# Optimization experiments

Measured on AMD Instinct MI355X. Metric: run time of the kernel, lower is better.

The kernel has to match this reference:

```python
import jax, jax.numpy as jnp
import numpy as np

T, N = 20, 32768          # seq_length, numNodes
D_IN, D_EMB, D_H, D_OUT = 2, 64, 128, 5


def setup_inputs() -> dict:
    key = jax.random.key(0)
    ks = jax.random.split(key, 12)
    s = 0.05
    return {
        "nodes": jax.random.normal(ks[0], (T, N, D_IN), jnp.float32),
        "present_mask": jax.random.randint(ks[1], (T, N), 0, 2).astype(bool),
        "hidden_states": jax.random.normal(ks[2], (N, D_H), jnp.float32),
        "cell_states": jax.random.normal(ks[3], (N, D_H), jnp.float32),
        "W_embed": jax.random.normal(ks[4], (D_IN, D_EMB), jnp.float32) * s,
        "b_embed": jnp.zeros((D_EMB,), jnp.float32),
        "W_ih": jax.random.normal(ks[5], (D_EMB, 4 * D_H), jnp.float32) * s,
        "b_ih": jnp.zeros((4 * D_H,), jnp.float32),
        "W_hh": jax.random.normal(ks[6], (D_H, 4 * D_H), jnp.float32) * s,
        "b_hh": jnp.zeros((4 * D_H,), jnp.float32),
        "W_out": jax.random.normal(ks[7], (D_H, D_OUT), jnp.float32) * s,
        "b_out": jnp.zeros((D_OUT,), jnp.float32),
    }


def reference(nodes, present_mask, hidden_states, cell_states,
              W_embed, b_embed, W_ih, b_ih, W_hh, b_hh, W_out, b_out):
    # Per-frame: gather present nodes -> embed+ReLU (dropout=eval identity)
    # -> LSTMCell -> scatter h/c/output back. Gather+scatter is expressed as
    # a masked update, which is mathematically identical.
    def step(carry, frame):
        h, c = carry
        x, mask = frame                      # x: [N,2], mask: [N]
        emb = jax.nn.relu(x @ W_embed + b_embed)              # [N,Demb]
        gates = emb @ W_ih + b_ih + h @ W_hh + b_hh           # [N,4H]
        i, f, g, o = jnp.split(gates, 4, axis=-1)             # torch order
        i, f, o = jax.nn.sigmoid(i), jax.nn.sigmoid(f), jax.nn.sigmoid(o)
        g = jnp.tanh(g)
        c_new = f * c + i * g
        h_new = o * jnp.tanh(c_new)
        m = mask[:, None]
        h = jnp.where(m, h_new, h)
        c = jnp.where(m, c_new, c)
        out = jnp.where(m, h_new @ W_out + b_out, 0.0)        # absent -> zeros
        return (h, c), out

    (h_fin, c_fin), outputs = jax.lax.scan(
        step, (hidden_states, cell_states), (nodes, present_mask))
    return outputs, h_fin, c_fin                              # [T,N,5],[N,H],[N,H]
```

## Files before the change

### kernel.cpp

```cpp
#include <hip/hip_runtime.h>
#include <cstddef>


typedef __attribute__((ext_vector_type(8))) short  s16x8;
typedef __attribute__((ext_vector_type(4))) float  f32x4;

namespace {
constexpr int T_STEPS = 20;
constexpr int NN      = 32768;
constexpr int D_EMB   = 64;
constexpr int D_H     = 128;
constexpr int D_OUT   = 5;
constexpr int G4      = 512;
constexpr int MT      = 64;
constexpr int BLOCK   = 512;
constexpr int GRID    = NN / MT;
constexpr int WP_ELEMS   = 8 * 4 * 6 * 64 * 8;
constexpr int WOUT_ELEMS = 4 * 64 * 8;
constexpr float LOG2E = 1.4426950408889634f;
constexpr float AM4   = -4.0f * LOG2E;
constexpr float AP2   =  2.0f * LOG2E;
constexpr float CINV  = 0.34657359027997264f;
constexpr size_t OFF_H = (size_t)T_STEPS * NN * D_OUT;
constexpr size_t OFF_C = OFF_H + (size_t)NN * D_H;
}

__device__ __forceinline__ unsigned short f2bf(float x) {
    unsigned u = __float_as_uint(x);
    u = (u + 0x7FFFu + ((u >> 16) & 1u)) >> 16;
    return (unsigned short)u;
}
__device__ __forceinline__ unsigned short f2bf_hw(float x) {
    __bf16 b = (__bf16)x;
    union { __bf16 b; unsigned short u; } cv;
    cv.b = b;
    return cv.u;
}
__device__ __forceinline__ float bf2f(unsigned short h) {
    return __uint_as_float(((unsigned)h) << 16);
}
__device__ __forceinline__ float exp2f_fast(float x) {
#if __has_builtin(__builtin_amdgcn_exp2f)
    return __builtin_amdgcn_exp2f(x);
#else
    return __expf(x * 0.6931471805599453f);
#endif
}
__device__ __forceinline__ float sig_pre(float a) {
    return __builtin_amdgcn_rcpf(1.0f + exp2f_fast(a));
}

__global__ void prepack_kernel(const float* __restrict__ W_ih,
                               const float* __restrict__ b_ih,
                               const float* __restrict__ W_hh,
                               const float* __restrict__ b_hh,
                               const float* __restrict__ W_out,
                               unsigned short* __restrict__ Wp,
                               unsigned short* __restrict__ WoutF,
                               float* __restrict__ b_sum) {
    int idx = blockIdx.x * blockDim.x + threadIdx.x;
    if (idx < WP_ELEMS) {
        int j    = idx & 7;
        int L    = (idx >> 3) & 63;
        int rest = idx >> 9;
        int kb   = rest % 6;
        int gw   = rest / 6;
        int g    = gw & 3, w = gw >> 2;
        int k    = kb * 32 + (L >> 4) * 8 + j;
        int col  = g * D_H + w * 16 + (L & 15);
        float v  = (k < D_EMB) ? W_ih[k * G4 + col] : W_hh[(k - D_EMB) * G4 + col];
        float s  = (g == 2) ? (2.0f * LOG2E) : (-LOG2E);
        Wp[idx] = f2bf(v * s);
    } else if (idx < WP_ELEMS + WOUT_ELEMS) {
        int i2 = idx - WP_ELEMS;
        int j = i2 & 7, L = (i2 >> 3) & 63, kb2 = i2 >> 9;
        int k = kb2 * 32 + (L >> 4) * 8 + j;
        int n = L & 15;
        WoutF[i2] = (n < D_OUT) ? f2bf(W_out[k * D_OUT + n]) : (unsigned short)0;
    }
    if (idx < G4) {
        int g = idx / D_H;
        float s = (g == 2) ? (2.0f * LOG2E) : (-LOG2E);
        b_sum[idx] = (b_ih[idx] + b_hh[idx]) * s;
    }
}

__global__ __launch_bounds__(BLOCK, 1) void vlstm_kernel(
    const float* __restrict__ nodes,
    const int*   __restrict__ mask,
    const float* __restrict__ h0,
    const float* __restrict__ c0,
    const float* __restrict__ W_embed,
    const float* __restrict__ b_embed,
    const float* __restrict__ b_out,
    const unsigned short* __restrict__ Wp,
    const unsigned short* __restrict__ WoutF,
    const float* __restrict__ b_sum,
    float* __restrict__ out)
{
    __shared__ __align__(16) unsigned short Acp[2][4 * 6 * 512];
    __shared__ __align__(16) unsigned short hNewC[2][4 * 4 * 512];
    __shared__ float          cS[MT * 132];
    __shared__ unsigned short hS[MT * 130];
    __shared__ float          st_o[2][MT * D_OUT];
    __shared__ __align__(16) unsigned short WoS[WOUT_ELEMS];
    __shared__ float We_s[2 * D_EMB];
    __shared__ float be_s[D_EMB];
    __shared__ unsigned long long msk64[2];
    __shared__ unsigned char lst[2][MT];
    __shared__ int nAs[2];

    const int tid  = threadIdx.x;
    const int wave = tid >> 6;
    const int L    = tid & 63;
    const int quad = L >> 4;
    const int l15  = L & 15;
    const int n_base = blockIdx.x * MT;
    const int u_lane = wave * 16 + l15;

    const unsigned short* wbase = Wp + (size_t)wave * (4 * 6 * 64 * 8);
    s16x8 Bf[4][6];
    #pragma unroll
    for (int g = 0; g < 4; g++)
        #pragma unroll
        for (int kb = 0; kb < 6; kb++)
            Bf[g][kb] = *(const s16x8*)(wbase + ((g * 6 + kb) * 64 + L) * 8);

    float bias[4];
    #pragma unroll
    for (int g = 0; g < 4; g++) bias[g] = b_sum[g * D_H + u_lane];
    const float bo = (l15 < D_OUT) ? b_out[l15] : 0.0f;

    const int kbu2 = u_lane >> 5;
    const int flg  = ((u_lane >> 3) & 3) * 128 + (u_lane & 7);
    const int j_u  = u_lane & 7;
    const int flh  = ((u_lane >> 3) & 3) * 128 + quad * 32;
    const int node_e = tid >> 3;
    const int eb     = tid & 7;

    for (int i = tid; i < 3 * D_EMB; i += BLOCK) {
        if (i < 2 * D_EMB) We_s[i] = W_embed[i];
        else               be_s[i - 2 * D_EMB] = b_embed[i - 2 * D_EMB];
    }
    for (int i = tid; i < WOUT_ELEMS; i += BLOCK) WoS[i] = WoutF[i];

    for (int i = tid; i < MT * D_H; i += BLOCK) {
        int node = i >> 7, u = i & 127;
        cS[node * 132 + u] = AP2 * c0[(size_t)(n_base + node) * D_H + u];
        hS[node * 130 + u] = f2bf_hw(h0[(size_t)(n_base + node) * D_H + u]);
    }
    if (wave == 0) {
        int lm0 = mask[n_base + L];
        unsigned long long bm = __ballot(lm0 != 0);
        int na     = __popcll(bm);
        int below  = __popcll(bm & ((1ull << L) - 1ull));
        int belowI = __popcll((~bm) & ((1ull << L) - 1ull));
        lst[0][lm0 ? below : (na + belowI)] = (unsigned char)L;
        if (L == 0) { msk64[0] = bm; nAs[0] = na; }
    }
    __syncthreads();

#define EMB_BUILD(B, XV, MN) do {                                              \
    if (((MN) >> node_e) & 1ull) {                                             \
        int j = __popcll((MN) & ((1ull << node_e) - 1ull));                    \
        s16x8 ev;                                                              \
        _Pragma("unroll")                                                      \
        for (int jj = 0; jj < 8; jj++) {                                       \
            int e = eb * 8 + jj;                                               \
            float v = fmaf((XV).x, We_s[e], fmaf((XV).y, We_s[D_EMB + e], be_s[e])); \
            ev[jj] = (short)f2bf_hw(fmaxf(v, 0.0f));                           \
        }                                                                      \
        *(s16x8*)(&Acp[B][((j >> 4) * 6 + (eb >> 2)) * 512 + (eb & 3) * 128 + (j & 15) * 8]) = ev; \
    } } while (0)

#define GATHER(B, LP, NAN_) do {                                               \
    for (int j = quad; j < (NAN_); j += 4) {                                   \
        int orig = (int)(LP)[j];                                               \
        Acp[B][((j >> 4) * 6 + 2 + kbu2) * 512 + flg + (j & 15) * 8] =         \
            hS[orig * 130 + u_lane];                                           \
    } } while (0)

    {
        float2 x0 = *(const float2*)(nodes + (size_t)(n_base + node_e) * 2);
        unsigned long long M0v = msk64[0];
        EMB_BUILD(0, x0, M0v);
        int nA0 = __builtin_amdgcn_readfirstlane(nAs[0]);
        GATHER(0, lst[0], nA0);
    }
    __syncthreads();

#define GEMM_RT(rt) do {                                                       \
    {   s16x8 af0 = *(const s16x8*)(Ar + ((rt) * 6 + 0) * 512 + L * 8);        \
        _Pragma("unroll")                                                      \
        for (int g = 0; g < 4; g++)                                            \
            acc[(rt) & 1][g] = __builtin_amdgcn_mfma_f32_16x16x32_bf16(        \
                af0, Bf[g][0], (f32x4){0.f, 0.f, 0.f, 0.f}, 0, 0, 0); }        \
    _Pragma("unroll")                                                          \
    for (int kb = 1; kb < 6; kb++) {                                           \
        s16x8 af = *(const s16x8*)(Ar + ((rt) * 6 + kb) * 512 + L * 8);        \
        _Pragma("unroll")                                                      \
        for (int g = 0; g < 4; g++)                                            \
            acc[(rt) & 1][g] = __builtin_amdgcn_mfma_f32_16x16x32_bf16(        \
                af, Bf[g][kb], acc[(rt) & 1][g], 0, 0, 0); }                   \
} while (0)

#define ACT_RT(rt) do {                                                        \
    _Pragma("unroll")                                                          \
    for (int r = 0; r < 4; r++) {                                              \
        int c    = (rt) * 16 + quad * 4 + r;                                   \
        int orig = (int)lstT[c];                                               \
        float cold = cS[orig * 132 + u_lane];                                  \
        float gi = sig_pre(acc[(rt) & 1][0][r] + bias[0]);                     \
        float gf = sig_pre(acc[(rt) & 1][1][r] + bias[1]);                     \
        float rg = sig_pre(acc[(rt) & 1][2][r] + bias[2]);                     \
        float go = sig_pre(acc[(rt) & 1][3][r] + bias[3]);                     \
        float ggL = fmaf(AM4, rg, AP2);                   \
        float cnL = fmaf(gf, cold, gi * ggL);             \
        float rr  = __builtin_amdgcn_rcpf(1.0f + exp2f_fast(cnL));             \
        float hv  = go * fmaf(-2.0f, rr, 1.0f);           \
        unsigned short hb = f2bf_hw(hv);                                       \
        if (c < nA) {                                                          \
            cS[orig * 132 + u_lane] = cnL;                                     \
            hS[orig * 130 + u_lane] = hb;                                      \
            hNc[((rt) * 4 + kbu2) * 512 + flh + r * 8 + j_u] = hb;             \
        }                                                                      \
    } } while (0)

    unsigned long long Mp = 0;
    int nAp = 0;

    for (int t = 0; t < T_STEPS; t++) {
        unsigned short* __restrict__ Ar   = Acp[t & 1];
        unsigned short* __restrict__ hNc  = hNewC[t & 1];
        const unsigned short* __restrict__ hPv = hNewC[(t + 1) & 1];
        const unsigned char*  __restrict__ lstT = lst[t & 1];

        const unsigned long long M = msk64[t & 1];
        const int nA  = __builtin_amdgcn_readfirstlane(nAs[t & 1]);
        const int ntA = (nA + 15) >> 4;

        float2 xv = make_float2(0.0f, 0.0f);
        if (t + 1 < T_STEPS) {
            xv = *(const float2*)(nodes + ((size_t)(t + 1) * NN + n_base + node_e) * 2);
            if (wave == 0) {
                int lm = mask[(size_t)(t + 1) * NN + n_base + L];
                unsigned long long bm = __ballot(lm != 0);
                int na     = __popcll(bm);
                int below  = __popcll(bm & ((1ull << L) - 1ull));
                int belowI = __popcll((~bm) & ((1ull << L) - 1ull));
                lst[(t + 1) & 1][lm ? below : (na + belowI)] = (unsigned char)L;
                if (L == 0) { msk64[(t + 1) & 1] = bm; nAs[(t + 1) & 1] = na; }
            }
        }

        f32x4 acc[2][4];
        if (ntA > 0) GEMM_RT(0);
        if (ntA > 1) GEMM_RT(1);
        if (ntA > 0) ACT_RT(0);
        if (ntA > 2) GEMM_RT(2);
        if (ntA > 1) ACT_RT(1);
        if (ntA > 3) GEMM_RT(3);
        if (ntA > 2) ACT_RT(2);
        if (t > 0) {
            int ntP = (nAp + 15) >> 4;
            if (wave < ntP) {
                f32x4 ao = (f32x4){0.f, 0.f, 0.f, 0.f};
                #pragma unroll
                for (int kb2 = 0; kb2 < 4; kb2++) {
                    s16x8 af = *(const s16x8*)(hPv + (wave * 4 + kb2) * 512 + L * 8);
                    s16x8 wf = *(const s16x8*)(WoS + (kb2 * 64 + L) * 8);
                    ao = __builtin_amdgcn_mfma_f32_16x16x32_bf16(af, wf, ao, 0, 0, 0);
                }
                if (l15 < D_OUT) {
                    #pragma unroll
                    for (int r = 0; r < 4; r++) {
                        int c = wave * 16 + quad * 4 + r;
                        st_o[(t - 1) & 1][c * D_OUT + l15] = ao[r] + bo;
                    }
                }
            }
        }
        if (ntA > 3) ACT_RT(3);
        __syncthreads();

        if (t > 0 && tid < MT * D_OUT) {
            int node = tid / D_OUT, d = tid - node * D_OUT;
            int act  = (int)((Mp >> node) & 1ull);
            int pos  = __popcll(Mp & ((1ull << node) - 1ull));
            float v  = act ? st_o[(t - 1) & 1][pos * D_OUT + d] : 0.0f;
            out[((size_t)(t - 1) * NN + n_base) * D_OUT + tid] = v;
        }
        if (t + 1 < T_STEPS) {
            unsigned long long Mn = msk64[(t + 1) & 1];
            EMB_BUILD((t + 1) & 1, xv, Mn);
            int nAn = __builtin_amdgcn_readfirstlane(nAs[(t + 1) & 1]);
            GATHER((t + 1) & 1, lst[(t + 1) & 1], nAn);
        }
        Mp = M; nAp = nA;
        __syncthreads();
    }

    {
        int ntP = (nAp + 15) >> 4;
        if (wave < ntP) {
            const unsigned short* hPv = hNewC[(T_STEPS - 1) & 1];
            f32x4 ao = (f32x4){0.f, 0.f, 0.f, 0.f};
            #pragma unroll
            for (int kb2 = 0; kb2 < 4; kb2++) {
                s16x8 af = *(const s16x8*)(hPv + (wave * 4 + kb2) * 512 + L * 8);
                s16x8 wf = *(const s16x8*)(WoS + (kb2 * 64 + L) * 8);
                ao = __builtin_amdgcn_mfma_f32_16x16x32_bf16(af, wf, ao, 0, 0, 0);
            }
            if (l15 < D_OUT) {
                #pragma unroll
                for (int r = 0; r < 4; r++) {
                    int c = wave * 16 + quad * 4 + r;
                    st_o[(T_STEPS - 1) & 1][c * D_OUT + l15] = ao[r] + bo;
                }
            }
        }
    }
    __syncthreads();
    if (tid < MT * D_OUT) {
        int node = tid / D_OUT, d = tid - node * D_OUT;
        int act  = (int)((Mp >> node) & 1ull);
        int pos  = __popcll(Mp & ((1ull << node) - 1ull));
        float v  = act ? st_o[(T_STEPS - 1) & 1][pos * D_OUT + d] : 0.0f;
        out[((size_t)(T_STEPS - 1) * NN + n_base) * D_OUT + tid] = v;
    }
    for (int i = tid; i < MT * D_H; i += BLOCK) {
        int node = i >> 7, u = i & 127;
        out[OFF_H + (size_t)(n_base + node) * D_H + u] = bf2f(hS[node * 130 + u]);
        out[OFF_C + (size_t)(n_base + node) * D_H + u] = CINV * cS[node * 132 + u];
    }

#undef EMB_BUILD
#undef GATHER
#undef GEMM_RT
#undef ACT_RT
}

extern "C" void kernel_launch(void* const* d_in, const int* in_sizes, int n_in,
                              void* d_out, int out_size, void* d_ws, size_t ws_size,
                              hipStream_t stream) {
    const float* nodes   = (const float*)d_in[0];
    const int*   mask    = (const int*)  d_in[1];
    const float* h0      = (const float*)d_in[2];
    const float* c0      = (const float*)d_in[3];
    const float* W_embed = (const float*)d_in[4];
    const float* b_embed = (const float*)d_in[5];
    const float* W_ih    = (const float*)d_in[6];
    const float* b_ih    = (const float*)d_in[7];
    const float* W_hh    = (const float*)d_in[8];
    const float* b_hh    = (const float*)d_in[9];
    const float* W_out   = (const float*)d_in[10];
    const float* b_out   = (const float*)d_in[11];
    float* out = (float*)d_out;

    unsigned short* Wp    = (unsigned short*)d_ws;
    unsigned short* WoutF = Wp + WP_ELEMS;
    float*          b_sum = (float*)(WoutF + WOUT_ELEMS);

    prepack_kernel<<<(WP_ELEMS + WOUT_ELEMS + 255) / 256, 256, 0, stream>>>(
        W_ih, b_ih, W_hh, b_hh, W_out, Wp, WoutF, b_sum);

    vlstm_kernel<<<GRID, BLOCK, 0, stream>>>(
        nodes, mask, h0, c0, W_embed, b_embed, b_out, Wp, WoutF, b_sum, out);
}
```

Baseline: 272.8 us.

## Read hidden state directly from padded LDS rows instead of gathering into A buffer

Removes the per-step GATHER pass that copied compacted hidden-state elements into a packed A-operand buffer. The GEMM now loads the hidden-state MFMA fragments straight from hS, using the active-node index list and a 16-byte-aligned row stride of 136. The new h values are held in registers and written back to hS after the barrier, which avoids a read/write race on hS. This cuts scalar LDS traffic and shrinks the A buffer, at the cost of indexed row loads and extra registers for the buffered h values.

```diff
diff --git a/kernel.cpp b/kernel.cpp
--- a/kernel.cpp
+++ b/kernel.cpp
@@ -17,6 +17,7 @@
 constexpr int GRID    = NN / MT;
 constexpr int WP_ELEMS   = 8 * 4 * 6 * 64 * 8;
 constexpr int WOUT_ELEMS = 4 * 64 * 8;
+constexpr int HSTR    = 136;
 constexpr float LOG2E = 1.4426950408889634f;
 constexpr float AM4   = -4.0f * LOG2E;
 constexpr float AP2   =  2.0f * LOG2E;
@@ -98,10 +99,10 @@
     const float* __restrict__ b_sum,
     float* __restrict__ out)
 {
-    __shared__ __align__(16) unsigned short Acp[2][4 * 6 * 512];
+    __shared__ __align__(16) unsigned short E[2][4 * 2 * 512];
     __shared__ __align__(16) unsigned short hNewC[2][4 * 4 * 512];
     __shared__ float          cS[MT * 132];
-    __shared__ unsigned short hS[MT * 130];
+    __shared__ __align__(16) unsigned short hS[MT * HSTR];
     __shared__ float          st_o[2][MT * D_OUT];
     __shared__ __align__(16) unsigned short WoS[WOUT_ELEMS];
     __shared__ float We_s[2 * D_EMB];
@@ -132,7 +133,6 @@
     const float bo = (l15 < D_OUT) ? b_out[l15] : 0.0f;
 
     const int kbu2 = u_lane >> 5;
-    const int flg  = ((u_lane >> 3) & 3) * 128 + (u_lane & 7);
     const int j_u  = u_lane & 7;
     const int flh  = ((u_lane >> 3) & 3) * 128 + quad * 32;
     const int node_e = tid >> 3;
@@ -146,8 +146,8 @@
 
     for (int i = tid; i < MT * D_H; i += BLOCK) {
         int node = i >> 7, u = i & 127;
-        cS[node * 132 + u] = AP2 * c0[(size_t)(n_base + node) * D_H + u];
-        hS[node * 130 + u] = f2bf_hw(h0[(size_t)(n_base + node) * D_H + u]);
+        cS[node * 132 + u]  = AP2 * c0[(size_t)(n_base + node) * D_H + u];
+        hS[node * HSTR + u] = f2bf_hw(h0[(size_t)(n_base + node) * D_H + u]);
     }
     if (wave == 0) {
         int lm0 = mask[n_base + L];
@@ -170,34 +170,32 @@
             float v = fmaf((XV).x, We_s[e], fmaf((XV).y, We_s[D_EMB + e], be_s[e])); \
             ev[jj] = (short)f2bf_hw(fmaxf(v, 0.0f));                           \
         }                                                                      \
-        *(s16x8*)(&Acp[B][((j >> 4) * 6 + (eb >> 2)) * 512 + (eb & 3) * 128 + (j & 15) * 8]) = ev; \
-    } } while (0)
-
-#define GATHER(B, LP, NAN_) do {                                               \
-    for (int j = quad; j < (NAN_); j += 4) {                                   \
-        int orig = (int)(LP)[j];                                               \
-        Acp[B][((j >> 4) * 6 + 2 + kbu2) * 512 + flg + (j & 15) * 8] =         \
-            hS[orig * 130 + u_lane];                                           \
+        *(s16x8*)(&E[B][((j >> 4) * 2 + (eb >> 2)) * 512 + (eb & 3) * 128 + (j & 15) * 8]) = ev; \
     } } while (0)
 
     {
         float2 x0 = *(const float2*)(nodes + (size_t)(n_base + node_e) * 2);
         unsigned long long M0v = msk64[0];
         EMB_BUILD(0, x0, M0v);
-        int nA0 = __builtin_amdgcn_readfirstlane(nAs[0]);
-        GATHER(0, lst[0], nA0);
     }
     __syncthreads();
 
 #define GEMM_RT(rt) do {                                                       \
-    {   s16x8 af0 = *(const s16x8*)(Ar + ((rt) * 6 + 0) * 512 + L * 8);        \
+    int og = (int)lstT[(rt) * 16 + l15];                                       \
+    const unsigned short* hrow = hS + og * HSTR + quad * 8;                    \
+    {   s16x8 af0 = *(const s16x8*)(Er + ((rt) * 2 + 0) * 512 + L * 8);        \
         _Pragma("unroll")                                                      \
         for (int g = 0; g < 4; g++)                                            \
             acc[(rt) & 1][g] = __builtin_amdgcn_mfma_f32_16x16x32_bf16(        \
                 af0, Bf[g][0], (f32x4){0.f, 0.f, 0.f, 0.f}, 0, 0, 0); }        \
+    {   s16x8 af1 = *(const s16x8*)(Er + ((rt) * 2 + 1) * 512 + L * 8);        \
+        _Pragma("unroll")                                                      \
+        for (int g = 0; g < 4; g++)                                            \
+            acc[(rt) & 1][g] = __builtin_amdgcn_mfma_f32_16x16x32_bf16(        \
+                af1, Bf[g][1], acc[(rt) & 1][g], 0, 0, 0); }                   \
     _Pragma("unroll")                                                          \
-    for (int kb = 1; kb < 6; kb++) {                                           \
-        s16x8 af = *(const s16x8*)(Ar + ((rt) * 6 + kb) * 512 + L * 8);        \
+    for (int kb = 2; kb < 6; kb++) {                                           \
+        s16x8 af = *(const s16x8*)(hrow + (kb - 2) * 32);                      \
         _Pragma("unroll")                                                      \
         for (int g = 0; g < 4; g++)                                            \
             acc[(rt) & 1][g] = __builtin_amdgcn_mfma_f32_16x16x32_bf16(        \
@@ -219,9 +217,9 @@
         float rr  = __builtin_amdgcn_rcpf(1.0f + exp2f_fast(cnL));             \
         float hv  = go * fmaf(-2.0f, rr, 1.0f);           \
         unsigned short hb = f2bf_hw(hv);                                       \
+        hbv[rt][r] = hb;                                                       \
         if (c < nA) {                                                          \
             cS[orig * 132 + u_lane] = cnL;                                     \
-            hS[orig * 130 + u_lane] = hb;                                      \
             hNc[((rt) * 4 + kbu2) * 512 + flh + r * 8 + j_u] = hb;             \
         }                                                                      \
     } } while (0)
@@ -230,7 +228,7 @@
     int nAp = 0;
 
     for (int t = 0; t < T_STEPS; t++) {
-        unsigned short* __restrict__ Ar   = Acp[t & 1];
+        unsigned short* __restrict__ Er   = E[t & 1];
         unsigned short* __restrict__ hNc  = hNewC[t & 1];
         const unsigned short* __restrict__ hPv = hNewC[(t + 1) & 1];
         const unsigned char*  __restrict__ lstT = lst[t & 1];
@@ -254,6 +252,7 @@
         }
 
         f32x4 acc[2][4];
+        unsigned short hbv[4][4];
         if (ntA > 0) GEMM_RT(0);
         if (ntA > 1) GEMM_RT(1);
         if (ntA > 0) ACT_RT(0);
@@ -283,6 +282,13 @@
         if (ntA > 3) ACT_RT(3);
         __syncthreads();
 
+        #pragma unroll
+        for (int rt = 0; rt < 4; rt++)
+            #pragma unroll
+            for (int r = 0; r < 4; r++) {
+                int c = rt * 16 + quad * 4 + r;
+                if (c < nA) hS[(int)lstT[c] * HSTR + u_lane] = hbv[rt][r];
+            }
         if (t > 0 && tid < MT * D_OUT) {
             int node = tid / D_OUT, d = tid - node * D_OUT;
             int act  = (int)((Mp >> node) & 1ull);
@@ -293,8 +299,6 @@
         if (t + 1 < T_STEPS) {
             unsigned long long Mn = msk64[(t + 1) & 1];
             EMB_BUILD((t + 1) & 1, xv, Mn);
-            int nAn = __builtin_amdgcn_readfirstlane(nAs[(t + 1) & 1]);
-            GATHER((t + 1) & 1, lst[(t + 1) & 1], nAn);
         }
         Mp = M; nAp = nA;
         __syncthreads();
@@ -330,12 +334,11 @@
     }
     for (int i = tid; i < MT * D_H; i += BLOCK) {
         int node = i >> 7, u = i & 127;
-        out[OFF_H + (size_t)(n_base + node) * D_H + u] = bf2f(hS[node * 130 + u]);
+        out[OFF_H + (size_t)(n_base + node) * D_H + u] = bf2f(hS[node * HSTR + u]);
         out[OFF_C + (size_t)(n_base + node) * D_H + u] = CINV * cS[node * 132 + u];
     }
 
 #undef EMB_BUILD
-#undef GATHER
 #undef GEMM_RT
 #undef ACT_RT
 }
```

New measurement: 270.2 us. No clear change (-0.9%).
